# Kernel tuning notes

Hardware: AMD Instinct MI355X
Metric: run time of the kernel (lower is better)

## Reference

```python
import jax, jax.numpy as jnp
import numpy as np

DIM = 512
NUM_HEADS = 8
HEAD_DIM = DIM // NUM_HEADS
FFN_DIM = 4 * DIM
EPS = 1e-6


def rmsnorm(x, w):
    rms = jnp.sqrt(jnp.mean(x * x, axis=-1, keepdims=True) + EPS)
    return x / rms * w


def setup_inputs() -> dict:
    key = jax.random.key(0)
    ks = jax.random.split(key, 8)
    B, T = 4, 2048
    x = jax.random.normal(ks[0], (B, T, DIM), dtype=jnp.float32)
    # Linear weights stored as [in, out] (transpose of torch layout)
    w_qkv = jax.random.normal(ks[1], (DIM, 3 * DIM), dtype=jnp.float32) * 0.02
    w_out = jax.random.normal(ks[2], (DIM, DIM), dtype=jnp.float32) * 0.02
    b_out = jnp.zeros((DIM,), dtype=jnp.float32)
    w1 = jax.random.normal(ks[3], (DIM, FFN_DIM), dtype=jnp.float32) * 0.02
    b1 = jnp.zeros((FFN_DIM,), dtype=jnp.float32)
    w2 = jax.random.normal(ks[4], (FFN_DIM, DIM), dtype=jnp.float32) * 0.02
    b2 = jnp.zeros((DIM,), dtype=jnp.float32)
    norm1_w = jnp.ones((DIM,), dtype=jnp.float32)
    norm2_w = jnp.ones((DIM,), dtype=jnp.float32)
    return {
        "x": x, "norm1_w": norm1_w, "norm2_w": norm2_w,
        "w_qkv": w_qkv, "w_out": w_out, "b_out": b_out,
        "w1": w1, "b1": b1, "w2": w2, "b2": b2,
        "context_size": 64,
    }


def reference(x, norm1_w, norm2_w, w_qkv, w_out, b_out, w1, b1, w2, b2, context_size):
    B, T, D = x.shape
    H, Hd = NUM_HEADS, HEAD_DIM
    # --- attention sublayer ---
    xn = rmsnorm(x, norm1_w)
    qkv = xn @ w_qkv                      # (B, T, 3D)
    q, k, v = jnp.split(qkv, 3, axis=-1)
    q = q.reshape(B, T, H, Hd).transpose(0, 2, 1, 3)  # (B, H, T, Hd)
    k = k.reshape(B, T, H, Hd).transpose(0, 2, 1, 3)
    v = v.reshape(B, T, H, Hd).transpose(0, 2, 1, 3)
    scale = Hd ** -0.5
    scores = jnp.einsum('bhqd,bhkd->bhqk', q, k) * scale  # (B, H, T, T)
    idx = jnp.arange(T)
    band = jnp.abs(idx[:, None] - idx[None, :]) <= context_size  # (T, T)
    scores = jnp.where(band[None, None], scores, -jnp.inf)
    attn = jax.nn.softmax(scores, axis=-1)
    out = jnp.einsum('bhqk,bhkd->bhqd', attn, v)  # (B, H, T, Hd)
    out = out.transpose(0, 2, 1, 3).reshape(B, T, D)
    out = out @ w_out + b_out
    x = x + out
    # --- FFN sublayer ---
    h = rmsnorm(x, norm2_w)
    h = jax.nn.gelu(h @ w1 + b1, approximate=False)
    x = x + (h @ w2 + b2)
    return x
```

## Files before the change

### kernel.cpp

```cpp
#include <hip/hip_runtime.h>
#include <cstdint>
#include <cstddef>

#define B_  4
#define T_  2048
#define D_  512
#define NH_ 8
#define HD_ 64
#define FF_ 2048
#define M_  (B_*T_)

typedef unsigned short u16;
typedef __attribute__((ext_vector_type(8))) unsigned short u16x8;
typedef __attribute__((ext_vector_type(8))) __bf16         bf16x8;
typedef __attribute__((ext_vector_type(4))) float          f32x4;

__device__ __forceinline__ u16 f2bf(float f) {
  unsigned u = __float_as_uint(f);
  u += 0x7FFF + ((u >> 16) & 1);
  return (u16)(u >> 16);
}
__device__ __forceinline__ float bf2f(u16 h) {
  return __uint_as_float((unsigned)h << 16);
}

__device__ __forceinline__ f32x4 mfma_bf16(u16x8 a, u16x8 b, f32x4 c) {
  return __builtin_amdgcn_mfma_f32_16x16x32_bf16(
      __builtin_bit_cast(bf16x8, a), __builtin_bit_cast(bf16x8, b), c, 0, 0, 0);
}

__device__ __forceinline__ void async16(const void* g, void* l) {
  __builtin_amdgcn_global_load_lds(
      (const __attribute__((address_space(1))) unsigned int*)g,
      (__attribute__((address_space(3))) unsigned int*)l, 16, 0, 0);
}

__device__ __forceinline__ float gelu_f(float v) {
  float ax = fabsf(v) * 0.70710678118f;
  float t = 1.0f / (1.0f + 0.3275911f * ax);
  float p = ((((1.061405429f * t - 1.453152027f) * t + 1.421413741f) * t
              - 0.284496736f) * t + 0.254829592f) * t;
  float e = __expf(-ax * ax);
  float er = 1.0f - p * e;
  float s = (v >= 0.0f) ? er : -er;
  return 0.5f * v * (1.0f + s);
}

__global__ __launch_bounds__(256) void prep_kernel(
    const float* __restrict__ i0, u16* __restrict__ o0,
    const float* __restrict__ i1, u16* __restrict__ o1,
    const float* __restrict__ i2, u16* __restrict__ o2,
    const float* __restrict__ i3, u16* __restrict__ o3,
    const float* __restrict__ x, const float* __restrict__ n1w,
    u16* __restrict__ xn, u16* __restrict__ xbf) {
  __shared__ float tile[32][33];
  const int bid = blockIdx.x, tid = threadIdx.x;
  if (bid < 3072) {
    const float* in; u16* out; int R, C, gx, lb;
    if (bid < 768)       { in = i0; out = o0; R = 512;  C = 1536; gx = 48; lb = bid; }
    else if (bid < 1024) { in = i1; out = o1; R = 512;  C = 512;  gx = 16; lb = bid - 768; }
    else if (bid < 2048) { in = i2; out = o2; R = 512;  C = 2048; gx = 64; lb = bid - 1024; }
    else                 { in = i3; out = o3; R = 2048; C = 512;  gx = 16; lb = bid - 2048; }
    int c0 = (lb % gx) * 32, r0 = (lb / gx) * 32;
    int tx = tid & 31, ty = tid >> 5;
#pragma unroll
    for (int i = 0; i < 4; i++)
      tile[ty + i * 8][tx] = in[(size_t)(r0 + ty + i * 8) * C + c0 + tx];
    __syncthreads();
#pragma unroll
    for (int i = 0; i < 4; i++)
      out[(size_t)(c0 + ty + i * 8) * R + r0 + tx] = f2bf(tile[tx][ty + i * 8]);
  } else {
    int row  = (bid - 3072) * 4 + (tid >> 6);
    int lane = tid & 63;
    const float* xr = x + (size_t)row * D_ + lane * 8;
    float v[8];
    *(float4*)(v)     = *(const float4*)xr;
    *(float4*)(v + 4) = *(const float4*)(xr + 4);
    u16 rw[8];
#pragma unroll
    for (int e = 0; e < 8; e++) rw[e] = f2bf(v[e]);
    *(uint4*)(xbf + (size_t)row * D_ + lane * 8) = *(uint4*)rw;
    float ss = 0.f;
#pragma unroll
    for (int e = 0; e < 8; e++) ss += v[e] * v[e];
#pragma unroll
    for (int m = 1; m < 64; m <<= 1) ss += __shfl_xor(ss, m, 64);
    float inv = rsqrtf(ss * (1.0f / D_) + 1e-6f);
    const float* wr = n1w + lane * 8;
    float wv[8];
    *(float4*)(wv)     = *(const float4*)wr;
    *(float4*)(wv + 4) = *(const float4*)(wr + 4);
    u16 o[8];
#pragma unroll
    for (int e = 0; e < 8; e++) o[e] = f2bf(v[e] * inv * wv[e]);
    *(uint4*)(xn + (size_t)row * D_ + lane * 8) = *(uint4*)o;
  }
}

__global__ __launch_bounds__(256) void rmsnorm_kernel(const u16* __restrict__ xv,
                                                      const float* __restrict__ w,
                                                      u16* __restrict__ out) {
  int row  = blockIdx.x * 4 + (threadIdx.x >> 6);
  int lane = threadIdx.x & 63;
  float v[8];
  u16x8 raw = *(const u16x8*)(xv + (size_t)row * D_ + lane * 8);
#pragma unroll
  for (int e = 0; e < 8; e++) v[e] = bf2f(raw[e]);
  float ss = 0.f;
#pragma unroll
  for (int e = 0; e < 8; e++) ss += v[e] * v[e];
#pragma unroll
  for (int m = 1; m < 64; m <<= 1) ss += __shfl_xor(ss, m, 64);
  float inv = rsqrtf(ss * (1.0f / D_) + 1e-6f);
  const float* wr = w + lane * 8;
  float wv[8];
  *(float4*)(wv)     = *(const float4*)wr;
  *(float4*)(wv + 4) = *(const float4*)(wr + 4);
  u16 o[8];
#pragma unroll
  for (int e = 0; e < 8; e++) o[e] = f2bf(v[e] * inv * wv[e]);
  *(uint4*)(out + (size_t)row * D_ + lane * 8) = *(uint4*)o;
}

template <int BM, int BN, bool HAS_BIAS, int RES_MODE, bool DO_GELU, bool STORE_BF16>
__global__ __launch_bounds__(256) void gemm_kernel(
    const u16* __restrict__ A, const u16* __restrict__ Bt, void* __restrict__ Cv,
    const float* __restrict__ bias, const void* __restrict__ resv,
    int M, int N, int K) {
  constexpr int ACH = BM / 32;
  constexpr int BCH = BN / 32;
  constexpr int WM  = BM / 2, WN = BN / 2;
  constexpr int MI  = WM / 16, NJ = WN / 16;
  constexpr int EW  = BN + 4;
  constexpr int STG = (BM + BN) * 128;
  constexpr int EPB = 32 * EW * 4;
  constexpr int SMB = (2 * STG > EPB) ? 2 * STG : EPB;
  __shared__ __align__(16) char smem[SMB];
  const int tid = threadIdx.x;
  const int lane = tid & 63, w = tid >> 6;
  const int quad = lane >> 4, m16 = lane & 15;
  const int wm = w & 1, wn = w >> 1;
  const int m0 = blockIdx.y * BM, n0 = blockIdx.x * BN;

  f32x4 acc[MI][NJ];
#pragma unroll
  for (int i = 0; i < MI; i++)
#pragma unroll
    for (int j = 0; j < NJ; j++) acc[i][j] = (f32x4){0.f, 0.f, 0.f, 0.f};

  const int srow = tid >> 3;
  const int scol = (((tid & 7) ^ (srow & 7))) * 8;
  const u16* Ag = A  + (size_t)(m0 + srow) * K + scol;
  const u16* Bg = Bt + (size_t)(n0 + srow) * K + scol;

  auto stage = [&](int buf, int kt) {
    char* base = smem + buf * STG;
#pragma unroll
    for (int c = 0; c < ACH; c++)
      async16(Ag + (size_t)c * 32 * K + kt, base + c * 4096 + tid * 16);
#pragma unroll
    for (int c = 0; c < BCH; c++)
      async16(Bg + (size_t)c * 32 * K + kt, base + BM * 128 + c * 4096 + tid * 16);
  };
  auto compute = [&](int buf) {
    const u16* lA = (const u16*)(smem + buf * STG);
    const u16* lB = (const u16*)(smem + buf * STG + BM * 128);
#pragma unroll
    for (int kk = 0; kk < 2; kk++) {
      const int sl = ((kk * 4 + quad) ^ (m16 & 7)) * 8;
      const u16* pa = lA + (wm * WM + m16) * 64 + sl;
      const u16* pb = lB + (wn * WN + m16) * 64 + sl;
      u16x8 af[MI], bfr[NJ];
#pragma unroll
      for (int i = 0; i < MI; i++) af[i] = *(const u16x8*)(pa + i * 1024);
#pragma unroll
      for (int j = 0; j < NJ; j++) bfr[j] = *(const u16x8*)(pb + j * 1024);
#pragma unroll
      for (int i = 0; i < MI; i++)
#pragma unroll
        for (int j = 0; j < NJ; j++)
          acc[i][j] = mfma_bf16(af[i], bfr[j], acc[i][j]);
    }
  };

  const int nk = K >> 6;
  stage(0, 0);
  for (int t = 0; t < nk; t++) {
    __syncthreads();
    if (t + 1 < nk) stage((t + 1) & 1, (t + 1) << 6);
    compute(t & 1);
  }

  float* eps = (float*)smem;
  constexpr int REPS = (32 * BN) / (256 * 8);
  float bv[REPS > 0 ? REPS : 1][8];
  if (HAS_BIAS) {
#pragma unroll
    for (int rep = 0; rep < REPS; rep++) {
      const int col = (BN == 128) ? ((tid & 15) * 8) : ((tid & 7) * 8);
      *(float4*)(bv[rep])     = *(const float4*)(bias + n0 + col);
      *(float4*)(bv[rep] + 4) = *(const float4*)(bias + n0 + col + 4);
    }
  }
#pragma unroll
  for (int i = 0; i < MI; i++) {
    __syncthreads();
#pragma unroll
    for (int j = 0; j < NJ; j++)
#pragma unroll
      for (int r = 0; r < 4; r++)
        eps[(wm * 16 + quad * 4 + r) * EW + wn * WN + j * 16 + m16] =
            acc[i][j][r];
    __syncthreads();
#pragma unroll
    for (int rep = 0; rep < REPS; rep++) {
      const int lr  = (BN == 128) ? (rep * 16 + (tid >> 4)) : (tid >> 3);
      const int col = (BN == 128) ? ((tid & 15) * 8) : ((tid & 7) * 8);
      const int rg  = m0 + (lr >> 4) * WM + i * 16 + (lr & 15);
      float v[8];
      *(float4*)(v)     = *(const float4*)(eps + lr * EW + col);
      *(float4*)(v + 4) = *(const float4*)(eps + lr * EW + col + 4);
      if (HAS_BIAS) {
#pragma unroll
        for (int e = 0; e < 8; e++) v[e] += bv[rep][e];
      }
      if (DO_GELU) {
#pragma unroll
        for (int e = 0; e < 8; e++) v[e] = gelu_f(v[e]);
      }
      const size_t idx = (size_t)rg * N + n0 + col;
      if (RES_MODE == 1) {
        float4 r0 = *(const float4*)((const float*)resv + idx);
        float4 r1 = *(const float4*)((const float*)resv + idx + 4);
        v[0] += r0.x; v[1] += r0.y; v[2] += r0.z; v[3] += r0.w;
        v[4] += r1.x; v[5] += r1.y; v[6] += r1.z; v[7] += r1.w;
      } else if (RES_MODE == 2) {
        u16x8 rr = *(const u16x8*)((const u16*)resv + idx);
#pragma unroll
        for (int e = 0; e < 8; e++) v[e] += bf2f(rr[e]);
      }
      if (STORE_BF16) {
        u16 o[8];
#pragma unroll
        for (int e = 0; e < 8; e++) o[e] = f2bf(v[e]);
        *(uint4*)((u16*)Cv + idx) = *(uint4*)o;
      } else {
        *(float4*)((float*)Cv + idx)     = *(float4*)(v);
        *(float4*)((float*)Cv + idx + 4) = *(float4*)(v + 4);
      }
    }
  }
}

#define VP_ 216
__global__ __launch_bounds__(256) void attn_kernel(const u16* __restrict__ qkv,
                                                   u16* __restrict__ out) {
  __shared__ __align__(16) char smem[26624 + 64 * VP_ * 2];
  u16* Ks = (u16*)smem;
  u16* Vt = (u16*)(smem + 26624);
  const int tid = threadIdx.x, lane = tid & 63, w = tid >> 6;
  const int quad = lane >> 4, m16 = lane & 15;
  const int q0 = blockIdx.x * 64, h = blockIdx.y, b = blockIdx.z;
  const int kstart = q0 - 64;
  const u16* base = qkv + (size_t)b * T_ * 1536;

  for (int c = tid; c < 1664; c += 256) {
    int row = c >> 3, ch = c & 7;
    int j = kstart + row;
    j = j < 0 ? 0 : (j > T_ - 1 ? T_ - 1 : j);
    *(uint4*)(Ks + row * 64 + ((ch ^ (row & 7)) * 8)) =
        *(const uint4*)(base + (size_t)j * 1536 + 512 + h * 64 + ch * 8);
  }
  for (int c = tid; c < 1664; c += 256) {
    int row = c >> 3, cc = (c & 7) * 8;
    int j = kstart + row;
    j = j < 0 ? 0 : (j > T_ - 1 ? T_ - 1 : j);
    uint4 u = *(const uint4*)(base + (size_t)j * 1536 + 1024 + h * 64 + cc);
    u16 tmp[8];
    *(uint4*)tmp = u;
#pragma unroll
    for (int i = 0; i < 8; i++) Vt[(cc + i) * VP_ + row] = tmp[i];
  }
  const int qw = q0 + w * 16;
  const u16* qb = base + (size_t)(qw + m16) * 1536 + h * 64 + quad * 8;
  u16x8 a0 = *(const u16x8*)qb;
  u16x8 a1 = *(const u16x8*)(qb + 32);
  __syncthreads();

  float s[10][4];
#pragma unroll
  for (int t = 0; t < 10; t++) {
    int kt = (w + t) * 16;
    int kr = kt + m16, sw = kr & 7;
    u16x8 kb0 = *(const u16x8*)(Ks + kr * 64 + ((quad ^ sw) * 8));
    u16x8 kb1 = *(const u16x8*)(Ks + kr * 64 + (((4 + quad) ^ sw) * 8));
    f32x4 acc = {0.f, 0.f, 0.f, 0.f};
    acc = mfma_bf16(a0, kb0, acc);
    acc = mfma_bf16(a1, kb1, acc);
    int jab = kstart + kt + m16;
#pragma unroll
    for (int r = 0; r < 4; r++) {
      int q = qw + quad * 4 + r;
      int d = q - jab;
      bool valid = (jab >= 0) && (jab < T_) && (d <= 64) && (d >= -64);
      s[t][r] = valid ? acc[r] * 0.125f : -1e30f;
    }
  }
  float mx[4], sm[4];
#pragma unroll
  for (int r = 0; r < 4; r++) mx[r] = -1e30f;
#pragma unroll
  for (int t = 0; t < 10; t++)
#pragma unroll
    for (int r = 0; r < 4; r++) mx[r] = fmaxf(mx[r], s[t][r]);
#pragma unroll
  for (int r = 0; r < 4; r++) {
#pragma unroll
    for (int msk = 1; msk < 16; msk <<= 1)
      mx[r] = fmaxf(mx[r], __shfl_xor(mx[r], msk, 64));
    sm[r] = 0.f;
  }
#pragma unroll
  for (int t = 0; t < 10; t++)
#pragma unroll
    for (int r = 0; r < 4; r++) {
      float e = __expf(s[t][r] - mx[r]);
      s[t][r] = e; sm[r] += e;
    }
#pragma unroll
  for (int r = 0; r < 4; r++) {
#pragma unroll
    for (int msk = 1; msk < 16; msk <<= 1) sm[r] += __shfl_xor(sm[r], msk, 64);
    sm[r] = 1.0f / sm[r];
  }
  __syncthreads();
  u16* Ps = (u16*)smem + w * 2688;
#pragma unroll
  for (int t = 0; t < 10; t++)
#pragma unroll
    for (int r = 0; r < 4; r++)
      Ps[(quad * 4 + r) * 168 + t * 16 + m16] = f2bf(s[t][r] * sm[r]);
  __syncthreads();

  f32x4 o[4];
#pragma unroll
  for (int dt = 0; dt < 4; dt++) o[dt] = (f32x4){0.f, 0.f, 0.f, 0.f};
#pragma unroll
  for (int c5 = 0; c5 < 5; c5++) {
    u16x8 pa = *(const u16x8*)(Ps + m16 * 168 + c5 * 32 + quad * 8);
#pragma unroll
    for (int dt = 0; dt < 4; dt++) {
      u16x8 vb = *(const u16x8*)(Vt + (dt * 16 + m16) * VP_ + w * 16 + c5 * 32 + quad * 8);
      o[dt] = mfma_bf16(pa, vb, o[dt]);
    }
  }
#pragma unroll
  for (int dt = 0; dt < 4; dt++)
#pragma unroll
    for (int r = 0; r < 4; r++)
      out[(size_t)(b * T_ + qw + quad * 4 + r) * D_ + h * HD_ + dt * 16 + m16] =
          f2bf(o[dt][r]);
}

extern "C" void kernel_launch(void* const* d_in, const int* in_sizes, int n_in,
                              void* d_out, int out_size, void* d_ws, size_t ws_size,
                              hipStream_t stream) {
  (void)in_sizes; (void)n_in; (void)out_size; (void)ws_size;
  const float* x     = (const float*)d_in[0];
  const float* n1w   = (const float*)d_in[1];
  const float* n2w   = (const float*)d_in[2];
  const float* w_qkv = (const float*)d_in[3];
  const float* w_out = (const float*)d_in[4];
  const float* b_out = (const float*)d_in[5];
  const float* w1    = (const float*)d_in[6];
  const float* b1    = (const float*)d_in[7];
  const float* w2    = (const float*)d_in[8];
  const float* b2    = (const float*)d_in[9];
  float* out = (float*)d_out;
  char* ws = (char*)d_ws;

  u16* wqkvT  = (u16*)(ws + 0);
  u16* woutT  = (u16*)(ws + 1572864);
  u16* w1T    = (u16*)(ws + 2097152);
  u16* w2T    = (u16*)(ws + 4194304);
  u16* xn     = (u16*)(ws + 6291456);
  u16* qkv    = (u16*)(ws + 14680064);
  u16* attno  = (u16*)(ws + 39845888);
  u16* x1     = (u16*)(ws + 48234496);
  u16* xbf    = (u16*)(ws + 56623104);
  u16* hn     = xn;
  u16* hbuf   = qkv;

  prep_kernel<<<5120, 256, 0, stream>>>(
      w_qkv, wqkvT, w_out, woutT, w1, w1T, w2, w2T, x, n1w, xn, xbf);

  gemm_kernel<64, 128, false, 0, false, true><<<dim3(12, 128), 256, 0, stream>>>(
      xn, wqkvT, (void*)qkv, nullptr, nullptr, M_, 3 * D_, D_);
  attn_kernel<<<dim3(32, 8, 4), 256, 0, stream>>>(qkv, attno);
  gemm_kernel<64, 128, true, 2, false, true><<<dim3(4, 128), 256, 0, stream>>>(
      attno, woutT, (void*)x1, b_out, xbf, M_, D_, D_);
  rmsnorm_kernel<<<2048, 256, 0, stream>>>(x1, n2w, hn);
  gemm_kernel<128, 128, true, 0, true, true><<<dim3(16, 64), 256, 0, stream>>>(
      hn, w1T, (void*)hbuf, b1, nullptr, M_, FF_, D_);
  gemm_kernel<64, 128, true, 2, false, false><<<dim3(4, 128), 256, 0, stream>>>(
      hbuf, w2T, (void*)out, b2, x1, M_, D_, FF_);
}
```

Measured before the change: 211.4 us.

## Fold RMSNorm into GEMMs via weight scaling and per-row epilogue scale

The norm weights are folded into the transposed QKV and W1 weights during prep. The prep kernel now writes only per-row inverse RMS values, and the QKV GEMM reads the raw bf16 x and applies that scale in its epilogue. The out-projection GEMM accumulates per-row sums of squares with atomics, so the FFN GEMM can compute the second norm scale itself, which removes the standalone rmsnorm kernel and the normalized-activation buffers. The attention grid is also remapped to interleave query chunks, and the atomics make the float summation order nondeterministic.

```diff
diff --git a/kernel.cpp b/kernel.cpp
--- a/kernel.cpp
+++ b/kernel.cpp
@@ -52,25 +52,27 @@
     const float* __restrict__ i2, u16* __restrict__ o2,
     const float* __restrict__ i3, u16* __restrict__ o3,
     const float* __restrict__ x, const float* __restrict__ n1w,
-    u16* __restrict__ xn, u16* __restrict__ xbf) {
+    const float* __restrict__ n2w,
+    float* __restrict__ inv, u16* __restrict__ xbf, float* __restrict__ ssz) {
   __shared__ float tile[32][33];
   const int bid = blockIdx.x, tid = threadIdx.x;
   if (bid < 3072) {
-    const float* in; u16* out; int R, C, gx, lb;
-    if (bid < 768)       { in = i0; out = o0; R = 512;  C = 1536; gx = 48; lb = bid; }
-    else if (bid < 1024) { in = i1; out = o1; R = 512;  C = 512;  gx = 16; lb = bid - 768; }
-    else if (bid < 2048) { in = i2; out = o2; R = 512;  C = 2048; gx = 64; lb = bid - 1024; }
-    else                 { in = i3; out = o3; R = 2048; C = 512;  gx = 16; lb = bid - 2048; }
+    const float* in; u16* out; const float* sc; int R, C, gx, lb;
+    if (bid < 768)       { in = i0; out = o0; R = 512;  C = 1536; gx = 48; lb = bid;        sc = n1w; }
+    else if (bid < 1024) { in = i1; out = o1; R = 512;  C = 512;  gx = 16; lb = bid - 768;  sc = nullptr; }
+    else if (bid < 2048) { in = i2; out = o2; R = 512;  C = 2048; gx = 64; lb = bid - 1024; sc = n2w; }
+    else                 { in = i3; out = o3; R = 2048; C = 512;  gx = 16; lb = bid - 2048; sc = nullptr; }
     int c0 = (lb % gx) * 32, r0 = (lb / gx) * 32;
     int tx = tid & 31, ty = tid >> 5;
 #pragma unroll
     for (int i = 0; i < 4; i++)
       tile[ty + i * 8][tx] = in[(size_t)(r0 + ty + i * 8) * C + c0 + tx];
     __syncthreads();
+    float s = sc ? sc[r0 + tx] : 1.0f;
 #pragma unroll
     for (int i = 0; i < 4; i++)
-      out[(size_t)(c0 + ty + i * 8) * R + r0 + tx] = f2bf(tile[tx][ty + i * 8]);
-  } else {
+      out[(size_t)(c0 + ty + i * 8) * R + r0 + tx] = f2bf(tile[tx][ty + i * 8] * s);
+  } else if (bid < 5120) {
     int row  = (bid - 3072) * 4 + (tid >> 6);
     int lane = tid & 63;
     const float* xr = x + (size_t)row * D_ + lane * 8;
@@ -86,47 +88,18 @@
     for (int e = 0; e < 8; e++) ss += v[e] * v[e];
 #pragma unroll
     for (int m = 1; m < 64; m <<= 1) ss += __shfl_xor(ss, m, 64);
-    float inv = rsqrtf(ss * (1.0f / D_) + 1e-6f);
-    const float* wr = n1w + lane * 8;
-    float wv[8];
-    *(float4*)(wv)     = *(const float4*)wr;
-    *(float4*)(wv + 4) = *(const float4*)(wr + 4);
-    u16 o[8];
-#pragma unroll
-    for (int e = 0; e < 8; e++) o[e] = f2bf(v[e] * inv * wv[e]);
-    *(uint4*)(xn + (size_t)row * D_ + lane * 8) = *(uint4*)o;
-  }
-}
-
-__global__ __launch_bounds__(256) void rmsnorm_kernel(const u16* __restrict__ xv,
-                                                      const float* __restrict__ w,
-                                                      u16* __restrict__ out) {
-  int row  = blockIdx.x * 4 + (threadIdx.x >> 6);
-  int lane = threadIdx.x & 63;
-  float v[8];
-  u16x8 raw = *(const u16x8*)(xv + (size_t)row * D_ + lane * 8);
-#pragma unroll
-  for (int e = 0; e < 8; e++) v[e] = bf2f(raw[e]);
-  float ss = 0.f;
-#pragma unroll
-  for (int e = 0; e < 8; e++) ss += v[e] * v[e];
-#pragma unroll
-  for (int m = 1; m < 64; m <<= 1) ss += __shfl_xor(ss, m, 64);
-  float inv = rsqrtf(ss * (1.0f / D_) + 1e-6f);
-  const float* wr = w + lane * 8;
-  float wv[8];
-  *(float4*)(wv)     = *(const float4*)wr;
-  *(float4*)(wv + 4) = *(const float4*)(wr + 4);
-  u16 o[8];
-#pragma unroll
-  for (int e = 0; e < 8; e++) o[e] = f2bf(v[e] * inv * wv[e]);
-  *(uint4*)(out + (size_t)row * D_ + lane * 8) = *(uint4*)o;
-}
-
-template <int BM, int BN, bool HAS_BIAS, int RES_MODE, bool DO_GELU, bool STORE_BF16>
+    if (lane == 0) inv[row] = rsqrtf(ss * (1.0f / D_) + 1e-6f);
+  } else {
+    ssz[(bid - 5120) * 256 + tid] = 0.f;
+  }
+}
+
+template <int BM, int BN, bool HAS_BIAS, int RES_MODE, bool DO_GELU,
+          bool STORE_BF16, int SCALE_MODE, bool EMIT_SS>
 __global__ __launch_bounds__(256) void gemm_kernel(
     const u16* __restrict__ A, const u16* __restrict__ Bt, void* __restrict__ Cv,
     const float* __restrict__ bias, const void* __restrict__ resv,
+    const float* __restrict__ rowscale, float* __restrict__ ssout,
     int M, int N, int K) {
   constexpr int ACH = BM / 32;
   constexpr int BCH = BN / 32;
@@ -221,6 +194,13 @@
       float v[8];
       *(float4*)(v)     = *(const float4*)(eps + lr * EW + col);
       *(float4*)(v + 4) = *(const float4*)(eps + lr * EW + col + 4);
+      if (SCALE_MODE != 0) {
+        float rs;
+        if (SCALE_MODE == 1) rs = rowscale[rg];
+        else                 rs = rsqrtf(rowscale[rg] * (1.0f / D_) + 1e-6f);
+#pragma unroll
+        for (int e = 0; e < 8; e++) v[e] *= rs;
+      }
       if (HAS_BIAS) {
 #pragma unroll
         for (int e = 0; e < 8; e++) v[e] += bv[rep][e];
@@ -240,6 +220,16 @@
 #pragma unroll
         for (int e = 0; e < 8; e++) v[e] += bf2f(rr[e]);
       }
+      if (EMIT_SS) {
+        float ps = 0.f;
+#pragma unroll
+        for (int e = 0; e < 8; e++) ps += v[e] * v[e];
+        ps += __shfl_xor(ps, 1, 64);
+        ps += __shfl_xor(ps, 2, 64);
+        ps += __shfl_xor(ps, 4, 64);
+        ps += __shfl_xor(ps, 8, 64);
+        if ((tid & 15) == 0) atomicAdd(ssout + rg, ps);
+      }
       if (STORE_BF16) {
         u16 o[8];
 #pragma unroll
@@ -261,7 +251,8 @@
   u16* Vt = (u16*)(smem + 26624);
   const int tid = threadIdx.x, lane = tid & 63, w = tid >> 6;
   const int quad = lane >> 4, m16 = lane & 15;
-  const int q0 = blockIdx.x * 64, h = blockIdx.y, b = blockIdx.z;
+  const int qc = ((blockIdx.x & 7) << 2) | (blockIdx.x >> 3);
+  const int q0 = qc * 64, h = blockIdx.y, b = blockIdx.z;
   const int kstart = q0 - 64;
   const u16* base = qkv + (size_t)b * T_ * 1536;
 
@@ -384,25 +375,28 @@
   u16* woutT  = (u16*)(ws + 1572864);
   u16* w1T    = (u16*)(ws + 2097152);
   u16* w2T    = (u16*)(ws + 4194304);
-  u16* xn     = (u16*)(ws + 6291456);
+  float* inv  = (float*)(ws + 6291456);
+  float* sums = (float*)(ws + 6324224);
   u16* qkv    = (u16*)(ws + 14680064);
   u16* attno  = (u16*)(ws + 39845888);
   u16* x1     = (u16*)(ws + 48234496);
   u16* xbf    = (u16*)(ws + 56623104);
-  u16* hn     = xn;
   u16* hbuf   = qkv;
 
-  prep_kernel<<<5120, 256, 0, stream>>>(
-      w_qkv, wqkvT, w_out, woutT, w1, w1T, w2, w2T, x, n1w, xn, xbf);
-
-  gemm_kernel<64, 128, false, 0, false, true><<<dim3(12, 128), 256, 0, stream>>>(
-      xn, wqkvT, (void*)qkv, nullptr, nullptr, M_, 3 * D_, D_);
+  prep_kernel<<<5152, 256, 0, stream>>>(
+      w_qkv, wqkvT, w_out, woutT, w1, w1T, w2, w2T, x, n1w, n2w, inv, xbf, sums);
+
+  gemm_kernel<64, 128, false, 0, false, true, 1, false>
+      <<<dim3(12, 128), 256, 0, stream>>>(
+      xbf, wqkvT, (void*)qkv, nullptr, nullptr, inv, nullptr, M_, 3 * D_, D_);
   attn_kernel<<<dim3(32, 8, 4), 256, 0, stream>>>(qkv, attno);
-  gemm_kernel<64, 128, true, 2, false, true><<<dim3(4, 128), 256, 0, stream>>>(
-      attno, woutT, (void*)x1, b_out, xbf, M_, D_, D_);
-  rmsnorm_kernel<<<2048, 256, 0, stream>>>(x1, n2w, hn);
-  gemm_kernel<128, 128, true, 0, true, true><<<dim3(16, 64), 256, 0, stream>>>(
-      hn, w1T, (void*)hbuf, b1, nullptr, M_, FF_, D_);
-  gemm_kernel<64, 128, true, 2, false, false><<<dim3(4, 128), 256, 0, stream>>>(
-      hbuf, w2T, (void*)out, b2, x1, M_, D_, FF_);
-}
+  gemm_kernel<64, 128, true, 2, false, true, 0, true>
+      <<<dim3(4, 128), 256, 0, stream>>>(
+      attno, woutT, (void*)x1, b_out, xbf, nullptr, sums, M_, D_, D_);
+  gemm_kernel<128, 128, true, 0, true, true, 2, false>
+      <<<dim3(16, 64), 256, 0, stream>>>(
+      x1, w1T, (void*)hbuf, b1, nullptr, sums, nullptr, M_, FF_, D_);
+  gemm_kernel<64, 128, true, 2, false, false, 0, false>
+      <<<dim3(4, 128), 256, 0, stream>>>(
+      hbuf, w2T, (void*)out, b2, x1, nullptr, nullptr, M_, D_, FF_);
+}
```

After: 208.1 us. Within noise of the previous version (-1.5%).
